# Performance work log

Hardware: AMD Instinct MI355X
Metric: run time of the kernel (lower is better)

The kernel has to match this reference:

```python
import jax, jax.numpy as jnp
import numpy as np

K_BITS = 8
QMAX = float(2 ** (K_BITS - 1) - 1)  # 127 for symmetric int8 fake quant
BN_EPS = 1e-5
RES_SCALE = 1.0


def _ste(v, q):
    # straight-through estimator: forward q, backward identity wrt v
    return v + jax.lax.stop_gradient(q - v)


def quant_act(x, alpha):
    # PAMS-style: clamp to learnable alpha, symmetric uniform fake-quant
    xc = jnp.clip(x, -alpha, alpha)
    scale = alpha / QMAX
    q = jnp.round(xc / scale) * scale
    return _ste(xc, q)


def quant_weight(w):
    # symmetric max-abs weight fake-quant
    scale = jnp.max(jnp.abs(w)) / QMAX
    q = jnp.clip(jnp.round(w / scale), -QMAX, QMAX) * scale
    return _ste(w, q)


def conv3x3(x, w):
    return jax.lax.conv_general_dilated(
        x, w, window_strides=(1, 1), padding=[(1, 1), (1, 1)],
        dimension_numbers=("NCHW", "OIHW", "NCHW"))


def batchnorm(x, gamma, beta):
    # training-mode BN: biased batch statistics over (N, H, W)
    mean = jnp.mean(x, axis=(0, 2, 3), keepdims=True)
    var = jnp.var(x, axis=(0, 2, 3), keepdims=True)
    xhat = (x - mean) * jax.lax.rsqrt(var + BN_EPS)
    return xhat * gamma[None, :, None, None] + beta[None, :, None, None]


def prelu(x, a):
    return jnp.where(x >= 0, x, a * x)


def setup_inputs() -> dict:
    key = jax.random.key(0)
    ks = jax.random.split(key, 4)
    C = 64
    identity = jax.random.normal(ks[0], (8, C, 192, 192), dtype=jnp.float32)
    # conv weights, default_init_weights scale 0.1 (kaiming-ish * 0.1)
    w1 = jax.random.normal(ks[1], (C, C, 3, 3), dtype=jnp.float32) * 0.1
    w2 = jax.random.normal(ks[2], (C, C, 3, 3), dtype=jnp.float32) * 0.1
    return {
        "identity": identity,
        "bits": jnp.ones((1,), jnp.float32),
        "f": jnp.ones((1,), jnp.float32),
        "bits_out": jnp.zeros((1,), jnp.float32),
        "w1": w1,
        "w2": w2,
        "alpha1": jnp.array(8.0, jnp.float32),
        "alpha2": jnp.array(8.0, jnp.float32),
        "gamma1": jnp.ones((C,), jnp.float32),
        "beta1": jnp.zeros((C,), jnp.float32),
        "gamma2": jnp.ones((C,), jnp.float32),
        "beta2": jnp.zeros((C,), jnp.float32),
        "prelu_a": jnp.array(0.25, jnp.float32),
        "shortcut": jnp.ones((1,), jnp.float32),
    }


def reference(identity, bits, f, bits_out, w1, w2, alpha1, alpha2,
              gamma1, beta1, gamma2, beta2, prelu_a, shortcut):
    # quant conv1: quantize input act + weights, 3x3 conv
    x = conv3x3(quant_act(identity, alpha1), quant_weight(w1))
    # PReLU then BN1 (module applies bn1(act(x)))
    x = batchnorm(prelu(x, prelu_a), gamma1, beta1)
    # quant conv2
    out = conv3x3(quant_act(x, alpha2), quant_weight(w2))
    out = batchnorm(out, gamma2, beta2)
    out = identity * shortcut + out * RES_SCALE
    return (out, bits, f, bits_out)
```

## Files before the change

### kernel.cpp

```cpp
#include <hip/hip_runtime.h>
#include <hip/hip_bf16.h>
#include <math.h>

#define CNUM   64
#define HH     192
#define WW     192
#define NBATCH 8
#define HWSZ   (HH * WW)
#define CHWSZ  (CNUM * HWSZ)
#define TOTALSZ ((size_t)NBATCH * CHWSZ)
#define QMAXF  127.0f
#define BNEPS  1e-5f
#define PW     194

typedef __attribute__((ext_vector_type(4))) int i32x4;

#define OFF_PK1    0
#define OFF_PK2    18432
#define OFF_STATS  36864
#define OFF_SUM1   36864
#define OFF_SSQ1   37120
#define OFF_SUM2   37376
#define OFF_SSQ2   37632
#define OFF_WMAX   37888
#define OFF_SW     37890
#define OFF_T2     38148
#define OFF_QB     (38148 + 9634816)

__device__ inline float bf2f(unsigned short u) {
    return __builtin_bit_cast(float, (unsigned)u << 16);
}

__global__ __launch_bounds__(256)
void wmax_kernel(const float* __restrict__ w1,
                 const float* __restrict__ w2,
                 unsigned* __restrict__ wmaxbits) {
    const int which = blockIdx.y;
    const float4* w4 = (const float4*)(which ? w2 : w1);
    const int b = (blockIdx.x * 256 + threadIdx.x) * 2;
    const float4 a = w4[b], c = w4[b + 1];
    float m = fmaxf(fmaxf(fmaxf(fabsf(a.x), fabsf(a.y)), fmaxf(fabsf(a.z), fabsf(a.w))),
                    fmaxf(fmaxf(fabsf(c.x), fabsf(c.y)), fmaxf(fabsf(c.z), fabsf(c.w))));
#pragma unroll
    for (int off = 1; off < 64; off <<= 1) m = fmaxf(m, __shfl_xor(m, off));
    if ((threadIdx.x & 63) == 0)
        atomicMax(wmaxbits + which, __builtin_bit_cast(unsigned, m));
}

__global__ __launch_bounds__(256)
void wpack_kernel(const float* __restrict__ w1,
                  const float* __restrict__ w2,
                  const unsigned* __restrict__ wmaxbits,
                  char* __restrict__ pk1,
                  char* __restrict__ pk2,
                  float* __restrict__ swout) {
    const int which = blockIdx.y;
    const float* w  = which ? w2 : w1;
    char*        pk = which ? pk2 : pk1;
    const float scale = __builtin_bit_cast(float, wmaxbits[which]) / QMAXF;
    if (blockIdx.x == 0 && threadIdx.x == 0) swout[which] = scale;
    const int i0 = (blockIdx.x * 256 + threadIdx.x) * 8;
#pragma unroll
    for (int k = 0; k < 8; ++k) {
        const int i = i0 + k;
        const int j   = i & 15;
        const int l   = (i >> 4) & 63;
        const int ocb = (i >> 10) & 3;
        const int t   = i >> 12;
        const int oc  = ocb * 16 + (l & 15);
        const int ic  = ((l >> 4) & 3) * 16 + j;
        float q = rintf(w[oc * 576 + ic * 9 + t] / scale);
        q = fminf(fmaxf(q, -QMAXF), QMAXF);
        pk[i] = (char)(int)q;
    }
}

template<int XFORM, int SWZOUT>
__global__ __launch_bounds__(256, 3)
void conv_mfma_kernel(const void* __restrict__ in_p,
                      const char* __restrict__ wpk,
                      const float* __restrict__ swp,
                      const float* __restrict__ alpha_p,
                      const float* __restrict__ slope_p,
                      const float* __restrict__ st_sum,
                      const float* __restrict__ st_ssq,
                      const float* __restrict__ st_gamma,
                      const float* __restrict__ st_beta,
                      unsigned short* __restrict__ outp,
                      unsigned short* __restrict__ out_swz,
                      float* __restrict__ sum_g,
                      float* __restrict__ ssq_g) {
    __shared__ __align__(16) char s_in[1584 * 16];
    __shared__ __align__(16) short sT[SWZOUT ? 4 * 64 * 40 : 8];
    __shared__ float sred[256], ssred[256];
    __shared__ float sab[(XFORM == 1) ? 128 : 4];

    const int tid = threadIdx.x;
    const int x0 = blockIdx.x * 64;
    const int y0 = blockIdx.y * 4;
    const int n  = blockIdx.z;

    const float alpha  = alpha_p[0];
    const float inv_qs = QMAXF / alpha;

    if (XFORM == 1) {
        if (tid < 64) {
            const float cnt = (float)(NBATCH * HWSZ);
            const float sm = st_sum[tid] + st_sum[64 + tid] + st_sum[128 + tid] + st_sum[192 + tid];
            const float sq = st_ssq[tid] + st_ssq[64 + tid] + st_ssq[128 + tid] + st_ssq[192 + tid];
            const float mean = sm / cnt;
            const float var  = sq / cnt - mean * mean;
            const float inv  = 1.0f / sqrtf(var + BNEPS);
            const float a = st_gamma[tid] * inv;
            sab[tid] = a;
            sab[64 + tid] = st_beta[tid] - mean * a;
        }
        __syncthreads();
        const unsigned short* qv = (const unsigned short*)in_p;
        const unsigned short* qb0 = qv + ((size_t)(n * PW + y0) * PW + x0) * 64;
#pragma unroll
        for (int k = 0; k < 7; ++k) {
            const int c = tid + k * 256;
            if (c < 1584) {
                const int r  = c / 264;
                const int w  = c - r * 264;
                const int x  = w >> 2, gp = w & 3;
                const int px = x0 + x, pyy = y0 + r;
                int4 val = make_int4(0, 0, 0, 0);
                if ((unsigned)(px - 1) < 192u && (unsigned)(pyy - 1) < 192u) {
                    const int g16 = gp ^ ((x >> 1) & 3);
                    const unsigned short* qp = qb0 + (size_t)r * (PW * 64) + (size_t)x * 64;
                    const int s0 = (2 * g16) ^ (px & 7);
                    const int4 v0 = *(const int4*)(qp + s0 * 8);
                    const int4 v1 = *(const int4*)(qp + (s0 ^ 1) * 8);
                    const unsigned short* u0 = (const unsigned short*)&v0;
                    const unsigned short* u1 = (const unsigned short*)&v1;
                    char vb[16];
#pragma unroll
                    for (int jj = 0; jj < 8; ++jj) {
                        const int ic = g16 * 16 + jj;
                        float xx0 = sab[ic] * bf2f(u0[jj]) + sab[64 + ic];
                        xx0 = fminf(fmaxf(xx0, -alpha), alpha);
                        vb[jj] = (char)(int)rintf(xx0 * inv_qs);
                    }
#pragma unroll
                    for (int jj = 0; jj < 8; ++jj) {
                        const int ic = g16 * 16 + 8 + jj;
                        float xx1 = sab[ic] * bf2f(u1[jj]) + sab[64 + ic];
                        xx1 = fminf(fmaxf(xx1, -alpha), alpha);
                        vb[8 + jj] = (char)(int)rintf(xx1 * inv_qs);
                    }
                    val = *(int4*)vb;
                }
                *(int4*)&s_in[c * 16] = val;
            }
        }
    } else {
        const float* inp = (const float*)in_p;
        const int xq  = tid & 15;
        const int icl = tid >> 4;
        const int g16 = icl >> 2;
        const int wsl = (icl & 3) * 4;
        const int nh  = (xq < 2) ? 2 : 1;
        for (int r = 0; r < 6; ++r) {
            const int gy = y0 - 1 + r;
            const bool rv = ((unsigned)gy < 192u);
            for (int half = 0; half < nh; ++half) {
                const int qi  = half ? (16 + xq) : xq;
                const int gxb = x0 - 4 + qi * 4;
                const bool qv = rv && (gxb >= 0) && (gxb + 3 < 192);
                float4 rr[4];
                if (qv) {
#pragma unroll
                    for (int p = 0; p < 4; ++p) {
                        const int ic = icl * 4 + p;
                        rr[p] = *(const float4*)(inp + ((size_t)n * CNUM + ic) * HWSZ
                                                 + (size_t)gy * WW + gxb);
                    }
                }
#pragma unroll
                for (int j = 0; j < 4; ++j) {
                    const int xl = gxb + j + 1 - x0;
                    if ((unsigned)xl <= 65u) {
                        unsigned pkw = 0;
                        if (qv) {
#pragma unroll
                            for (int p = 0; p < 4; ++p) {
                                const float* rv4 = (const float*)&rr[p];
                                float v = fminf(fmaxf(rv4[j], -alpha), alpha);
                                v = rintf(v * inv_qs);
                                pkw |= ((unsigned)(unsigned char)(char)(int)v) << (8 * p);
                            }
                        }
                        const int gran = (r * 66 + xl) * 4 + (g16 ^ ((xl >> 1) & 3));
                        *(unsigned*)&s_in[gran * 16 + wsl] = pkw;
                    }
                }
            }
        }
    }
    __syncthreads();

    const int wave  = tid >> 6;
    const int lane  = tid & 63;
    const int xlane = lane & 15;
    const int icgl  = lane >> 4;

    i32x4 acc[4][4];
#pragma unroll
    for (int m = 0; m < 4; ++m)
#pragma unroll
        for (int nb = 0; nb < 4; ++nb) acc[m][nb] = (i32x4){0, 0, 0, 0};

#pragma unroll
    for (int t = 0; t < 9; ++t) {
        const int ky = t / 3, kx = t % 3;
        const int r = wave + ky;
        i32x4 bfrag[4], afrag[4];
        const char* bp = wpk + ((size_t)(t * 4) * 64 + lane) * 16;
#pragma unroll
        for (int nb = 0; nb < 4; ++nb) bfrag[nb] = *(const i32x4*)(bp + (size_t)nb * 1024);
#pragma unroll
        for (int m = 0; m < 4; ++m) {
            const int x = m * 16 + xlane + kx;
            afrag[m] = *(const i32x4*)&s_in[(size_t)((r * 66 + x) * 4 + (icgl ^ ((x >> 1) & 3))) * 16];
        }
#pragma unroll
        for (int m = 0; m < 4; ++m)
#pragma unroll
            for (int nb = 0; nb < 4; ++nb)
                acc[m][nb] = __builtin_amdgcn_mfma_i32_16x16x64_i8(
                    afrag[m], bfrag[nb], acc[m][nb], 0, 0, 0);
    }

    const float sfin  = (alpha / QMAXF) * swp[0];
    const float slope = slope_p ? slope_p[0] : 1.0f;
    const int gy  = y0 + wave;
    const int gx0 = x0 + icgl * 4;

    if (SWZOUT) {
#pragma unroll
        for (int h = 0; h < 2; ++h) {
#pragma unroll
            for (int nbi = 0; nbi < 2; ++nbi) {
                const int nb = 2 * h + nbi;
                const int oc = nb * 16 + xlane;
                float s = 0.0f, ss = 0.0f;
#pragma unroll
                for (int m = 0; m < 4; ++m) {
#pragma unroll
                    for (int rgi = 0; rgi < 4; ++rgi) {
                        float a = (float)acc[m][nb][rgi] * sfin;
                        a = (a >= 0.0f) ? a : slope * a;
                        s += a;
                        ss += a * a;
                        const int pxl = m * 16 + icgl * 4 + rgi;
                        sT[(wave * 64 + pxl) * 40 + (nbi * 16 + xlane)] =
                            (short)__builtin_bit_cast(unsigned short, __float2bfloat16(a));
                    }
                }
                s  += __shfl_xor(s, 16);  s  += __shfl_xor(s, 32);
                ss += __shfl_xor(ss, 16); ss += __shfl_xor(ss, 32);
                if (icgl == 0) { sred[wave * 64 + oc] = s; ssred[wave * 64 + oc] = ss; }
            }
            __syncthreads();
            {
                const int py = gy + 1;
                unsigned short* qrow = out_swz + ((size_t)n * PW + py) * (PW * 64);
#pragma unroll
                for (int kk = 0; kk < 4; ++kk) {
                    const int idx = kk * 64 + lane;
                    const int xx  = idx >> 2;
                    const int gg  = idx & 3;
                    const int g8  = h * 4 + gg;
                    const int px  = x0 + 1 + xx;
                    const int slot = g8 ^ (px & 7);
                    *(int4*)(qrow + (size_t)px * 64 + slot * 8) =
                        *(const int4*)&sT[(wave * 64 + xx) * 40 + gg * 8];
                }
            }
            __syncthreads();
        }
    } else {
#pragma unroll
        for (int nb = 0; nb < 4; ++nb) {
            const int oc = nb * 16 + xlane;
            float s = 0.0f, ss = 0.0f;
#pragma unroll
            for (int m = 0; m < 4; ++m) {
                float v[4];
#pragma unroll
                for (int rgi = 0; rgi < 4; ++rgi) {
                    float a = (float)acc[m][nb][rgi] * sfin;
                    a = (a >= 0.0f) ? a : slope * a;
                    v[rgi] = a;
                    s += a;
                    ss += a * a;
                }
                ushort4 pk;
                pk.x = __builtin_bit_cast(unsigned short, __float2bfloat16(v[0]));
                pk.y = __builtin_bit_cast(unsigned short, __float2bfloat16(v[1]));
                pk.z = __builtin_bit_cast(unsigned short, __float2bfloat16(v[2]));
                pk.w = __builtin_bit_cast(unsigned short, __float2bfloat16(v[3]));
                *(ushort4*)&outp[(size_t)(n * CNUM + oc) * HWSZ + (size_t)gy * WW + gx0 + m * 16] = pk;
            }
            s  += __shfl_xor(s, 16);  s  += __shfl_xor(s, 32);
            ss += __shfl_xor(ss, 16); ss += __shfl_xor(ss, 32);
            if (icgl == 0) { sred[wave * 64 + oc] = s; ssred[wave * 64 + oc] = ss; }
        }
        __syncthreads();
    }

    const int bank = (blockIdx.y ^ blockIdx.z) & 3;
    if (tid < 64) {
        atomicAdd(sum_g + bank * 64 + tid,
                  sred[tid] + sred[64 + tid] + sred[128 + tid] + sred[192 + tid]);
    } else if (tid < 128) {
        const int c = tid - 64;
        atomicAdd(ssq_g + bank * 64 + c,
                  ssred[c] + ssred[64 + c] + ssred[128 + c] + ssred[192 + c]);
    }
}

__global__ __launch_bounds__(256)
void final_kernel(const float* __restrict__ identity,
                  const unsigned short* __restrict__ t2,
                  const float* __restrict__ st_sum,
                  const float* __restrict__ st_ssq,
                  const float* __restrict__ st_gamma,
                  const float* __restrict__ st_beta,
                  const float* __restrict__ shortcut_p,
                  const float* __restrict__ bits,
                  const float* __restrict__ f,
                  const float* __restrict__ bits_out,
                  float* __restrict__ out) {
    __shared__ float sab[128];
    if (threadIdx.x < 64) {
        const int c = threadIdx.x;
        const float cnt = (float)(NBATCH * HWSZ);
        const float sm = st_sum[c] + st_sum[64 + c] + st_sum[128 + c] + st_sum[192 + c];
        const float sq = st_ssq[c] + st_ssq[64 + c] + st_ssq[128 + c] + st_ssq[192 + c];
        const float mean = sm / cnt;
        const float var  = sq / cnt - mean * mean;
        const float inv  = 1.0f / sqrtf(var + BNEPS);
        const float a = st_gamma[c] * inv;
        sab[c] = a;
        sab[64 + c] = st_beta[c] - mean * a;
    }
    __syncthreads();

    const size_t base = (size_t)blockIdx.x * 1024;
    const int   cch  = (int)((base / (HWSZ / 4)) % CNUM);
    const float a  = sab[cch];
    const float bb = sab[64 + cch];
    const float sc = shortcut_p[0];

    float4  idv[4];
    ushort4 tv[4];
#pragma unroll
    for (int k = 0; k < 4; ++k) {
        const size_t i4 = base + (size_t)k * 256 + threadIdx.x;
        idv[k] = ((const float4*)identity)[i4];
        tv[k]  = ((const ushort4*)t2)[i4];
    }
#pragma unroll
    for (int k = 0; k < 4; ++k) {
        const size_t i4 = base + (size_t)k * 256 + threadIdx.x;
        float4 o;
        o.x = idv[k].x * sc + a * bf2f(tv[k].x) + bb;
        o.y = idv[k].y * sc + a * bf2f(tv[k].y) + bb;
        o.z = idv[k].z * sc + a * bf2f(tv[k].z) + bb;
        o.w = idv[k].w * sc + a * bf2f(tv[k].w) + bb;
        ((float4*)out)[i4] = o;
    }
    if (blockIdx.x == 0 && threadIdx.x == 0) {
        out[TOTALSZ + 0] = bits[0];
        out[TOTALSZ + 1] = f[0];
        out[TOTALSZ + 2] = bits_out[0];
    }
}

extern "C" void kernel_launch(void* const* d_in, const int* in_sizes, int n_in,
                              void* d_out, int out_size, void* d_ws, size_t ws_size,
                              hipStream_t stream) {
    const float* identity = (const float*)d_in[0];
    const float* bits     = (const float*)d_in[1];
    const float* f        = (const float*)d_in[2];
    const float* bits_out = (const float*)d_in[3];
    const float* w1       = (const float*)d_in[4];
    const float* w2       = (const float*)d_in[5];
    const float* alpha1   = (const float*)d_in[6];
    const float* alpha2   = (const float*)d_in[7];
    const float* gamma1   = (const float*)d_in[8];
    const float* beta1    = (const float*)d_in[9];
    const float* gamma2   = (const float*)d_in[10];
    const float* beta2    = (const float*)d_in[11];
    const float* prelu_a  = (const float*)d_in[12];
    const float* shortcut = (const float*)d_in[13];
    float* out = (float*)d_out;
    float* ws  = (float*)d_ws;

    char*     pk1   = (char*)(ws + OFF_PK1);
    char*     pk2   = (char*)(ws + OFF_PK2);
    float*    sum1  = ws + OFF_SUM1;
    float*    ssq1  = ws + OFF_SSQ1;
    float*    sum2  = ws + OFF_SUM2;
    float*    ssq2  = ws + OFF_SSQ2;
    unsigned* wmaxb = (unsigned*)(ws + OFF_WMAX);
    float*    sw    = ws + OFF_SW;
    unsigned short* qb = (unsigned short*)(ws + OFF_QB);
    unsigned short* t2 = (unsigned short*)(ws + OFF_T2);

    hipMemsetAsync(ws + OFF_STATS, 0, 1026 * sizeof(float), stream);
    hipLaunchKernelGGL(wmax_kernel, dim3(18, 2), dim3(256), 0, stream, w1, w2, wmaxb);
    hipLaunchKernelGGL(wpack_kernel, dim3(18, 2), dim3(256), 0, stream,
                       w1, w2, wmaxb, pk1, pk2, sw);
    hipLaunchKernelGGL((conv_mfma_kernel<2, 1>), dim3(3, HH / 4, NBATCH), dim3(256), 0, stream,
                       (const void*)identity, pk1, sw + 0, alpha1, prelu_a,
                       (const float*)nullptr, (const float*)nullptr,
                       (const float*)nullptr, (const float*)nullptr,
                       (unsigned short*)nullptr, qb, sum1, ssq1);
    hipLaunchKernelGGL((conv_mfma_kernel<1, 0>), dim3(3, HH / 4, NBATCH), dim3(256), 0, stream,
                       (const void*)qb, pk2, sw + 1, alpha2, (const float*)nullptr,
                       sum1, ssq1, gamma1, beta1,
                       t2, (unsigned short*)nullptr, sum2, ssq2);
    hipLaunchKernelGGL(final_kernel, dim3((unsigned)(TOTALSZ / 4 / 1024)), dim3(256), 0, stream,
                       identity, t2, sum2, ssq2, gamma2, beta2,
                       shortcut, bits, f, bits_out, out);
}
```

Before: 252.4 us.

## Halve conv block row tile, split output channels across waves, raise occupancy

The conv tile shrinks from 4 output rows to 2 per block, and each wave now computes half of the 64 output channels (2 of 4 MFMA column blocks) instead of all channels for one row. This halves accumulator registers and LDS use, and the transpose buffer reuses the input LDS region, so launch bounds go from 3 to 5 blocks per CU. The LDS swizzle pattern also changes. In exchange the input halo is reloaded more often (4 rows per 2 output rows, against 6 per 4), each A fragment is reused across fewer MFMAs, and the grid doubles.

```diff
diff --git a/kernel.cpp b/kernel.cpp
--- a/kernel.cpp
+++ b/kernel.cpp
@@ -12,6 +12,7 @@
 #define QMAXF  127.0f
 #define BNEPS  1e-5f
 #define PW     194
+#define NGRAN  1056
 
 typedef __attribute__((ext_vector_type(4))) int i32x4;
 
@@ -30,6 +31,7 @@
 __device__ inline float bf2f(unsigned short u) {
     return __builtin_bit_cast(float, (unsigned)u << 16);
 }
+__device__ inline int FSW(int x) { return (x >> 2) & 3; }
 
 __global__ __launch_bounds__(256)
 void wmax_kernel(const float* __restrict__ w1,
@@ -76,7 +78,7 @@
 }
 
 template<int XFORM, int SWZOUT>
-__global__ __launch_bounds__(256, 3)
+__global__ __launch_bounds__(256, 5)
 void conv_mfma_kernel(const void* __restrict__ in_p,
                       const char* __restrict__ wpk,
                       const float* __restrict__ swp,
@@ -90,14 +92,13 @@
                       unsigned short* __restrict__ out_swz,
                       float* __restrict__ sum_g,
                       float* __restrict__ ssq_g) {
-    __shared__ __align__(16) char s_in[1584 * 16];
-    __shared__ __align__(16) short sT[SWZOUT ? 4 * 64 * 40 : 8];
-    __shared__ float sred[256], ssred[256];
+    __shared__ __align__(16) char s_in[SWZOUT ? 20480 : 16896];
+    __shared__ float sred[128], ssred[128];
     __shared__ float sab[(XFORM == 1) ? 128 : 4];
 
     const int tid = threadIdx.x;
     const int x0 = blockIdx.x * 64;
-    const int y0 = blockIdx.y * 4;
+    const int y0 = blockIdx.y * 2;
     const int n  = blockIdx.z;
 
     const float alpha  = alpha_p[0];
@@ -119,16 +120,16 @@
         const unsigned short* qv = (const unsigned short*)in_p;
         const unsigned short* qb0 = qv + ((size_t)(n * PW + y0) * PW + x0) * 64;
 #pragma unroll
-        for (int k = 0; k < 7; ++k) {
+        for (int k = 0; k < 5; ++k) {
             const int c = tid + k * 256;
-            if (c < 1584) {
+            if (c < NGRAN) {
                 const int r  = c / 264;
                 const int w  = c - r * 264;
                 const int x  = w >> 2, gp = w & 3;
                 const int px = x0 + x, pyy = y0 + r;
                 int4 val = make_int4(0, 0, 0, 0);
                 if ((unsigned)(px - 1) < 192u && (unsigned)(pyy - 1) < 192u) {
-                    const int g16 = gp ^ ((x >> 1) & 3);
+                    const int g16 = gp ^ FSW(x);
                     const unsigned short* qp = qb0 + (size_t)r * (PW * 64) + (size_t)x * 64;
                     const int s0 = (2 * g16) ^ (px & 7);
                     const int4 v0 = *(const int4*)(qp + s0 * 8);
@@ -162,7 +163,7 @@
         const int g16 = icl >> 2;
         const int wsl = (icl & 3) * 4;
         const int nh  = (xq < 2) ? 2 : 1;
-        for (int r = 0; r < 6; ++r) {
+        for (int r = 0; r < 4; ++r) {
             const int gy = y0 - 1 + r;
             const bool rv = ((unsigned)gy < 192u);
             for (int half = 0; half < nh; ++half) {
@@ -192,7 +193,7 @@
                                 pkw |= ((unsigned)(unsigned char)(char)(int)v) << (8 * p);
                             }
                         }
-                        const int gran = (r * 66 + xl) * 4 + (g16 ^ ((xl >> 1) & 3));
+                        const int gran = (r * 66 + xl) * 4 + (g16 ^ FSW(xl));
                         *(unsigned*)&s_in[gran * 16 + wsl] = pkw;
                     }
                 }
@@ -205,97 +206,91 @@
     const int lane  = tid & 63;
     const int xlane = lane & 15;
     const int icgl  = lane >> 4;
-
-    i32x4 acc[4][4];
+    const int row   = wave >> 1;
+    const int nbh   = wave & 1;
+
+    i32x4 acc[4][2];
 #pragma unroll
     for (int m = 0; m < 4; ++m)
 #pragma unroll
-        for (int nb = 0; nb < 4; ++nb) acc[m][nb] = (i32x4){0, 0, 0, 0};
+        for (int j = 0; j < 2; ++j) acc[m][j] = (i32x4){0, 0, 0, 0};
 
 #pragma unroll
     for (int t = 0; t < 9; ++t) {
         const int ky = t / 3, kx = t % 3;
-        const int r = wave + ky;
-        i32x4 bfrag[4], afrag[4];
-        const char* bp = wpk + ((size_t)(t * 4) * 64 + lane) * 16;
-#pragma unroll
-        for (int nb = 0; nb < 4; ++nb) bfrag[nb] = *(const i32x4*)(bp + (size_t)nb * 1024);
+        const int r = row + ky;
+        i32x4 bfrag[2], afrag[4];
+        const char* bp = wpk + ((size_t)(t * 4 + nbh * 2) * 64 + lane) * 16;
+        bfrag[0] = *(const i32x4*)(bp);
+        bfrag[1] = *(const i32x4*)(bp + 1024);
 #pragma unroll
         for (int m = 0; m < 4; ++m) {
             const int x = m * 16 + xlane + kx;
-            afrag[m] = *(const i32x4*)&s_in[(size_t)((r * 66 + x) * 4 + (icgl ^ ((x >> 1) & 3))) * 16];
+            afrag[m] = *(const i32x4*)&s_in[(size_t)((r * 66 + x) * 4 + (icgl ^ FSW(x))) * 16];
         }
 #pragma unroll
         for (int m = 0; m < 4; ++m)
 #pragma unroll
-            for (int nb = 0; nb < 4; ++nb)
-                acc[m][nb] = __builtin_amdgcn_mfma_i32_16x16x64_i8(
-                    afrag[m], bfrag[nb], acc[m][nb], 0, 0, 0);
+            for (int j = 0; j < 2; ++j)
+                acc[m][j] = __builtin_amdgcn_mfma_i32_16x16x64_i8(
+                    afrag[m], bfrag[j], acc[m][j], 0, 0, 0);
     }
 
     const float sfin  = (alpha / QMAXF) * swp[0];
     const float slope = slope_p ? slope_p[0] : 1.0f;
-    const int gy  = y0 + wave;
+    const int gy  = y0 + row;
     const int gx0 = x0 + icgl * 4;
 
+    float st_s[2]  = {0.f, 0.f};
+    float st_ss[2] = {0.f, 0.f};
+
     if (SWZOUT) {
-#pragma unroll
-        for (int h = 0; h < 2; ++h) {
-#pragma unroll
-            for (int nbi = 0; nbi < 2; ++nbi) {
-                const int nb = 2 * h + nbi;
-                const int oc = nb * 16 + xlane;
-                float s = 0.0f, ss = 0.0f;
-#pragma unroll
-                for (int m = 0; m < 4; ++m) {
-#pragma unroll
-                    for (int rgi = 0; rgi < 4; ++rgi) {
-                        float a = (float)acc[m][nb][rgi] * sfin;
-                        a = (a >= 0.0f) ? a : slope * a;
-                        s += a;
-                        ss += a * a;
-                        const int pxl = m * 16 + icgl * 4 + rgi;
-                        sT[(wave * 64 + pxl) * 40 + (nbi * 16 + xlane)] =
-                            (short)__builtin_bit_cast(unsigned short, __float2bfloat16(a));
-                    }
-                }
-                s  += __shfl_xor(s, 16);  s  += __shfl_xor(s, 32);
-                ss += __shfl_xor(ss, 16); ss += __shfl_xor(ss, 32);
-                if (icgl == 0) { sred[wave * 64 + oc] = s; ssred[wave * 64 + oc] = ss; }
-            }
-            __syncthreads();
-            {
-                const int py = gy + 1;
-                unsigned short* qrow = out_swz + ((size_t)n * PW + py) * (PW * 64);
-#pragma unroll
-                for (int kk = 0; kk < 4; ++kk) {
-                    const int idx = kk * 64 + lane;
-                    const int xx  = idx >> 2;
-                    const int gg  = idx & 3;
-                    const int g8  = h * 4 + gg;
-                    const int px  = x0 + 1 + xx;
-                    const int slot = g8 ^ (px & 7);
-                    *(int4*)(qrow + (size_t)px * 64 + slot * 8) =
-                        *(const int4*)&sT[(wave * 64 + xx) * 40 + gg * 8];
+        __syncthreads();
+        short* sT = (short*)s_in;
+        const int wbase = wave * 2560;
+        const int py = gy + 1;
+        unsigned short* qrow = out_swz + ((size_t)n * PW + py) * (PW * 64);
+#pragma unroll
+        for (int nb2 = 0; nb2 < 2; ++nb2) {
+#pragma unroll
+            for (int m = 0; m < 4; ++m) {
+#pragma unroll
+                for (int rgi = 0; rgi < 4; ++rgi) {
+                    float a = (float)acc[m][nb2][rgi] * sfin;
+                    a = (a >= 0.0f) ? a : slope * a;
+                    st_s[nb2]  += a;
+                    st_ss[nb2] += a * a;
+                    const int pxl = m * 16 + icgl * 4 + rgi;
+                    sT[wbase + pxl * 40 + nb2 * 16 + xlane] =
+                        (short)__builtin_bit_cast(unsigned short, __float2bfloat16(a));
                 }
             }
-            __syncthreads();
+        }
+#pragma unroll
+        for (int kk = 0; kk < 4; ++kk) {
+            const int idx = kk * 64 + lane;
+            const int xx  = idx >> 2;
+            const int gg  = idx & 3;
+            const int g8  = nbh * 4 + gg;
+            const int px  = x0 + 1 + xx;
+            const int slot = g8 ^ (px & 7);
+            *(int4*)(qrow + (size_t)px * 64 + slot * 8) =
+                *(const int4*)&sT[wbase + xx * 40 + gg * 8];
         }
     } else {
 #pragma unroll
-        for (int nb = 0; nb < 4; ++nb) {
-            const int oc = nb * 16 + xlane;
-            float s = 0.0f, ss = 0.0f;
+        for (int nb2 = 0; nb2 < 2; ++nb2) {
+            const int oc = nbh * 32 + nb2 * 16 + xlane;
 #pragma unroll
             for (int m = 0; m < 4; ++m) {
                 float v[4];
 #pragma unroll
                 for (int rgi = 0; rgi < 4; ++rgi) {
-                    float a = (float)acc[m][nb][rgi] * sfin;
+                    float a = (float)acc[m][nb2][rgi] * sfin;
                     a = (a >= 0.0f) ? a : slope * a;
                     v[rgi] = a;
-                    s += a;
-                    ss += a * a;
+                    st_s[nb2]  += a;
+                    st_ss[nb2] += a * a;
                 }
                 ushort4 pk;
                 pk.x = __builtin_bit_cast(unsigned short, __float2bfloat16(v[0]));
@@ -304,21 +299,30 @@
                 pk.w = __builtin_bit_cast(unsigned short, __float2bfloat16(v[3]));
                 *(ushort4*)&outp[(size_t)(n * CNUM + oc) * HWSZ + (size_t)gy * WW + gx0 + m * 16] = pk;
             }
-            s  += __shfl_xor(s, 16);  s  += __shfl_xor(s, 32);
-            ss += __shfl_xor(ss, 16); ss += __shfl_xor(ss, 32);
-            if (icgl == 0) { sred[wave * 64 + oc] = s; ssred[wave * 64 + oc] = ss; }
-        }
-        __syncthreads();
-    }
-
+        }
+    }
+
+#pragma unroll
+    for (int nb2 = 0; nb2 < 2; ++nb2) {
+        float s = st_s[nb2], ss = st_ss[nb2];
+        s  += __shfl_xor(s, 16);  s  += __shfl_xor(s, 32);
+        ss += __shfl_xor(ss, 16); ss += __shfl_xor(ss, 32);
+        if (icgl == 0) {
+            sred[wave * 32 + nb2 * 16 + xlane]  = s;
+            ssred[wave * 32 + nb2 * 16 + xlane] = ss;
+        }
+    }
+    __syncthreads();
     const int bank = (blockIdx.y ^ blockIdx.z) & 3;
     if (tid < 64) {
+        const int nb_c = tid >> 5, col = tid & 31;
         atomicAdd(sum_g + bank * 64 + tid,
-                  sred[tid] + sred[64 + tid] + sred[128 + tid] + sred[192 + tid]);
+                  sred[nb_c * 32 + col] + sred[(2 + nb_c) * 32 + col]);
     } else if (tid < 128) {
         const int c = tid - 64;
+        const int nb_c = c >> 5, col = c & 31;
         atomicAdd(ssq_g + bank * 64 + c,
-                  ssred[c] + ssred[64 + c] + ssred[128 + c] + ssred[192 + c]);
+                  ssred[nb_c * 32 + col] + ssred[(2 + nb_c) * 32 + col]);
     }
 }
 
@@ -415,12 +419,12 @@
     hipLaunchKernelGGL(wmax_kernel, dim3(18, 2), dim3(256), 0, stream, w1, w2, wmaxb);
     hipLaunchKernelGGL(wpack_kernel, dim3(18, 2), dim3(256), 0, stream,
                        w1, w2, wmaxb, pk1, pk2, sw);
-    hipLaunchKernelGGL((conv_mfma_kernel<2, 1>), dim3(3, HH / 4, NBATCH), dim3(256), 0, stream,
+    hipLaunchKernelGGL((conv_mfma_kernel<2, 1>), dim3(3, HH / 2, NBATCH), dim3(256), 0, stream,
                        (const void*)identity, pk1, sw + 0, alpha1, prelu_a,
                        (const float*)nullptr, (const float*)nullptr,
                        (const float*)nullptr, (const float*)nullptr,
                        (unsigned short*)nullptr, qb, sum1, ssq1);
-    hipLaunchKernelGGL((conv_mfma_kernel<1, 0>), dim3(3, HH / 4, NBATCH), dim3(256), 0, stream,
+    hipLaunchKernelGGL((conv_mfma_kernel<1, 0>), dim3(3, HH / 2, NBATCH), dim3(256), 0, stream,
                        (const void*)qb, pk2, sw + 1, alpha2, (const float*)nullptr,
                        sum1, ssq1, gamma1, beta1,
                        t2, (unsigned short*)nullptr, sum2, ssq2);
```

Measured after the change: 255.4 us. Within noise of the previous version (+1.2%).
